# Performance work log

Measured on AMD Instinct MI355X. Metric: run time of the kernel, lower is better.

## Reference

```python
import jax, jax.numpy as jnp
import numpy as np

B, T, C = 4, 4096, 512
H, KS = 8, 9
D = C // H
PAD = KS // 2


def setup_inputs() -> dict:
    key = jax.random.key(0)
    ks = jax.random.split(key, 9)
    s = 1.0 / np.sqrt(C)
    return {
        "x": jax.random.normal(ks[0], (B, T, C), jnp.float32),
        "Wq": jax.random.normal(ks[1], (C, C), jnp.float32) * s,
        "bq": jax.random.normal(ks[2], (C,), jnp.float32) * 0.01,
        "Wk": jax.random.normal(ks[3], (C, C), jnp.float32) * s,
        "bk": jax.random.normal(ks[4], (C,), jnp.float32) * 0.01,
        "Wv": jax.random.normal(ks[5], (C, C), jnp.float32) * s,
        "bv": jax.random.normal(ks[6], (C,), jnp.float32) * 0.01,
        "Wo": jax.random.normal(ks[7], (C, C), jnp.float32) * s,
        "bo": jax.random.normal(ks[8], (C,), jnp.float32) * 0.01,
    }


def reference(x, Wq, bq, Wk, bk, Wv, bv, Wo, bo):
    Bx, Tx, Cx = x.shape
    # projections (torch Linear: x @ W.T + b), split heads -> (B,H,T,D)
    q = (x @ Wq.T + bq).reshape(Bx, Tx, H, D).transpose(0, 2, 1, 3)
    k = (x @ Wk.T + bk).reshape(Bx, Tx, H, D).transpose(0, 2, 1, 3)
    v = (x @ Wv.T + bv).reshape(Bx, Tx, H, D).transpose(0, 2, 1, 3)
    # replicate-pad along time (matches F.pad mode='replicate')
    k_pad = jnp.pad(k, ((0, 0), (0, 0), (PAD, PAD), (0, 0)), mode='edge')
    v_pad = jnp.pad(v, ((0, 0), (0, 0), (PAD, PAD), (0, 0)), mode='edge')
    # window gather indices: (T, KS) into padded time axis
    idx = jnp.arange(Tx)[:, None] + jnp.arange(KS)[None, :]
    k_unf = k_pad[:, :, idx, :]  # (B,H,T,KS,D)
    v_unf = v_pad[:, :, idx, :]  # (B,H,T,KS,D)
    scale = 1.0 / np.sqrt(D)
    scores = jnp.einsum('bhtd,bhtkd->bhtk', q, k_unf) * scale  # (B,H,T,KS)
    attn = jax.nn.softmax(scores, axis=-1)
    y = jnp.einsum('bhtk,bhtkd->bhtd', attn, v_unf)  # (B,H,T,D)
    y = y.transpose(0, 2, 1, 3).reshape(Bx, Tx, Cx)
    return y @ Wo.T + bo
```

## Files before the change

### kernel.cpp

```cpp
#include <hip/hip_runtime.h>
#include <hip/hip_bf16.h>

#define B_    4
#define T_    4096
#define C_    512
#define H_    8
#define D_    64
#define KS_   9
#define PAD_  4
#define MTOT  (B_ * T_)
#define PLANE (MTOT * C_)
#define WU    (C_ * C_ / 8)

typedef __bf16 bf16_t;
typedef __bf16 bf16x8 __attribute__((ext_vector_type(8)));
typedef float  f32x4  __attribute__((ext_vector_type(4)));

__global__ __launch_bounds__(256)
void conv_w(const float* __restrict__ Wq, const float* __restrict__ Wk,
            const float* __restrict__ Wv, const float* __restrict__ Wo,
            bf16_t* __restrict__ dst) {
  int i = blockIdx.x * 256 + threadIdx.x;
  int w = i >> 15;
  const float* W = (w == 0) ? Wq : (w == 1) ? Wk : (w == 2) ? Wv : Wo;
  const float* s = W + (size_t)(i & (WU - 1)) * 8;
  float4 f0 = ((const float4*)s)[0];
  float4 f1 = ((const float4*)s)[1];
  bf16x8 o;
  o[0] = (bf16_t)f0.x; o[1] = (bf16_t)f0.y; o[2] = (bf16_t)f0.z; o[3] = (bf16_t)f0.w;
  o[4] = (bf16_t)f1.x; o[5] = (bf16_t)f1.y; o[6] = (bf16_t)f1.z; o[7] = (bf16_t)f1.w;
  ((bf16x8*)dst)[i] = o;
}

__global__ __launch_bounds__(256, 2)
void qkv_gemm(const float* __restrict__ x, const bf16_t* __restrict__ Wb,
              const float* __restrict__ bq, const float* __restrict__ bk,
              const float* __restrict__ bv, bf16_t* __restrict__ qkv) {
  __shared__ __align__(16) bf16_t lsA[128 * 32];
  __shared__ __align__(16) bf16_t lsB[3][128 * 32];

  const int tid  = threadIdx.x;
  const int lane = tid & 63;
  const int wave = tid >> 6;
  const int wm   = (wave >> 1) * 64;
  const int wn   = (wave & 1) * 64;
  const int m0   = blockIdx.y * 128;
  const int n0   = blockIdx.x * 128;

  f32x4 acc[3][4][4] = {};

  for (int k0 = 0; k0 < C_; k0 += 32) {
    bf16x8 a[2];
#pragma unroll
    for (int s = 0; s < 2; ++s) {
      int u = s * 256 + tid;
      int row = u >> 2, slot = u & 3;
      int c = slot ^ ((row >> 1) & 3);
      const float* src = x + (size_t)(m0 + row) * C_ + k0 + c * 8;
      float4 f0 = ((const float4*)src)[0];
      float4 f1 = ((const float4*)src)[1];
      a[s][0] = (bf16_t)f0.x; a[s][1] = (bf16_t)f0.y;
      a[s][2] = (bf16_t)f0.z; a[s][3] = (bf16_t)f0.w;
      a[s][4] = (bf16_t)f1.x; a[s][5] = (bf16_t)f1.y;
      a[s][6] = (bf16_t)f1.z; a[s][7] = (bf16_t)f1.w;
    }

    __syncthreads();
    *(bf16x8*)&lsA[(size_t)tid * 8]         = a[0];
    *(bf16x8*)&lsA[(size_t)(tid + 256) * 8] = a[1];
#pragma unroll
    for (int z = 0; z < 3; ++z)
#pragma unroll
      for (int s = 0; s < 2; ++s) {
        int u = s * 256 + tid;
        int row = u >> 2, slot = u & 3;
        int c = slot ^ ((row >> 1) & 3);
        const bf16_t* gb = Wb + (size_t)z * C_ * C_ +
                           (size_t)(n0 + row) * C_ + k0 + c * 8;
        __builtin_amdgcn_global_load_lds(
            (const __attribute__((address_space(1))) unsigned int*)gb,
            (__attribute__((address_space(3))) unsigned int*)&lsB[z][u * 8],
            16, 0, 0);
      }
    __syncthreads();

    const int rr = lane & 15;
    const int q  = lane >> 4;
    const int sl = (q ^ ((rr >> 1) & 3)) << 3;
    bf16x8 af[4];
#pragma unroll
    for (int i = 0; i < 4; ++i)
      af[i] = *(const bf16x8*)&lsA[(wm + i * 16 + rr) * 32 + sl];
#pragma unroll
    for (int z = 0; z < 3; ++z) {
      bf16x8 bfr[4];
#pragma unroll
      for (int j = 0; j < 4; ++j)
        bfr[j] = *(const bf16x8*)&lsB[z][(wn + j * 16 + rr) * 32 + sl];
#pragma unroll
      for (int i = 0; i < 4; ++i)
#pragma unroll
        for (int j = 0; j < 4; ++j)
          acc[z][i][j] = __builtin_amdgcn_mfma_f32_16x16x32_bf16(
              af[i], bfr[j], acc[z][i][j], 0, 0, 0);
    }
  }

  const int cn = lane & 15;
  const int rb = (lane >> 4) << 2;
  const int bb = m0 >> 12;
  const int hh = (n0 + wn) >> 6;
#pragma unroll
  for (int z = 0; z < 3; ++z) {
    const float* bias = (z == 0) ? bq : (z == 1) ? bk : bv;
    float bvals[4];
#pragma unroll
    for (int j = 0; j < 4; ++j) bvals[j] = bias[n0 + wn + j * 16 + cn];
    bf16_t* hb = qkv + (size_t)z * PLANE + (size_t)(bb * H_ + hh) * T_ * D_;
#pragma unroll
    for (int i = 0; i < 4; ++i) {
#pragma unroll
      for (int r = 0; r < 4; ++r) {
        int t = (m0 + wm + i * 16 + rb + r) & (T_ - 1);
        bf16_t* row = hb + (size_t)t * D_;
#pragma unroll
        for (int j = 0; j < 4; ++j)
          row[j * 16 + cn] = (bf16_t)(acc[z][i][j][r] + bvals[j]);
      }
    }
  }
}

__global__ __launch_bounds__(256, 2)
void out_gemm(const bf16_t* __restrict__ y, const bf16_t* __restrict__ Wob,
              const float* __restrict__ bo, float* __restrict__ out) {
  __shared__ __align__(16) bf16_t lsA[128 * 32];
  __shared__ __align__(16) bf16_t lsB[128 * 32];

  const int tid  = threadIdx.x;
  const int lane = tid & 63;
  const int wave = tid >> 6;
  const int wm   = (wave >> 1) * 64;
  const int wn   = (wave & 1) * 64;
  const int m0   = blockIdx.y * 128;
  const int n0   = blockIdx.x * 128;

  f32x4 acc[4][4] = {};

  for (int k0 = 0; k0 < C_; k0 += 32) {
    __syncthreads();
#pragma unroll
    for (int s = 0; s < 2; ++s) {
      int u = s * 256 + tid;
      int row = u >> 2, slot = u & 3;
      int c = slot ^ ((row >> 1) & 3);
      int m = m0 + row;
      int b = m >> 12, t = m & (T_ - 1);
      int h = k0 >> 6, d0 = (k0 & 63) + c * 8;
      const bf16_t* ga = y + (((size_t)(b * H_ + h) * T_ + t) * D_ + d0);
      const bf16_t* gb = Wob + (size_t)(n0 + row) * C_ + k0 + c * 8;
      __builtin_amdgcn_global_load_lds(
          (const __attribute__((address_space(1))) unsigned int*)ga,
          (__attribute__((address_space(3))) unsigned int*)&lsA[u * 8], 16, 0, 0);
      __builtin_amdgcn_global_load_lds(
          (const __attribute__((address_space(1))) unsigned int*)gb,
          (__attribute__((address_space(3))) unsigned int*)&lsB[u * 8], 16, 0, 0);
    }
    __syncthreads();

    const int rr = lane & 15;
    const int q  = lane >> 4;
    const int sl = (q ^ ((rr >> 1) & 3)) << 3;
    bf16x8 af[4], bfr[4];
#pragma unroll
    for (int i = 0; i < 4; ++i) {
      af[i]  = *(const bf16x8*)&lsA[(wm + i * 16 + rr) * 32 + sl];
      bfr[i] = *(const bf16x8*)&lsB[(wn + i * 16 + rr) * 32 + sl];
    }
#pragma unroll
    for (int i = 0; i < 4; ++i)
#pragma unroll
      for (int j = 0; j < 4; ++j)
        acc[i][j] = __builtin_amdgcn_mfma_f32_16x16x32_bf16(af[i], bfr[j],
                                                            acc[i][j], 0, 0, 0);
  }

  const int cn = lane & 15;
  const int rb = (lane >> 4) << 2;
  float bvals[4];
#pragma unroll
  for (int j = 0; j < 4; ++j) bvals[j] = bo[n0 + wn + j * 16 + cn];
#pragma unroll
  for (int i = 0; i < 4; ++i) {
#pragma unroll
    for (int r = 0; r < 4; ++r) {
      int gm = m0 + wm + i * 16 + rb + r;
      float* orow = out + (size_t)gm * C_ + (n0 + wn);
#pragma unroll
      for (int j = 0; j < 4; ++j)
        orow[j * 16 + cn] = acc[i][j][r] + bvals[j];
    }
  }
}

__global__ __launch_bounds__(256)
void attn_kernel(const bf16_t* __restrict__ qkv, bf16_t* __restrict__ y) {
  const int tid  = threadIdx.x;
  const int sub  = tid & 7;
  const int tl   = tid >> 3;
  const int t    = blockIdx.x * 32 + tl;
  const int h    = blockIdx.y;
  const int b    = blockIdx.z;

  const size_t pl = (size_t)(b * H_ + h) * T_ * D_;
  const bf16_t* q = qkv + pl;
  const bf16_t* k = qkv + (size_t)PLANE + pl;
  const bf16_t* v = qkv + (size_t)2 * PLANE + pl;
  const int c = sub * 8;

  int tj[KS_];
#pragma unroll
  for (int j = 0; j < KS_; ++j) {
    int tt = t - PAD_ + j;
    tj[j] = tt < 0 ? 0 : (tt >= T_ ? T_ - 1 : tt);
  }

  bf16x8 q8 = *(const bf16x8*)(q + (size_t)t * D_ + c);
  float qf[8];
#pragma unroll
  for (int e = 0; e < 8; ++e) qf[e] = (float)q8[e];

  float s[KS_];
#pragma unroll
  for (int j = 0; j < KS_; ++j) {
    bf16x8 k8 = *(const bf16x8*)(k + (size_t)tj[j] * D_ + c);
    float d0 = 0.f;
#pragma unroll
    for (int e = 0; e < 8; ++e) d0 += qf[e] * (float)k8[e];
    s[j] = d0;
  }

#pragma unroll
  for (int m = 1; m < 8; m <<= 1)
#pragma unroll
    for (int j = 0; j < KS_; ++j) s[j] += __shfl_xor(s[j], m, 8);

  float mx = s[0];
#pragma unroll
  for (int j = 1; j < KS_; ++j) mx = fmaxf(mx, s[j]);
  float w[KS_], sum = 0.f;
#pragma unroll
  for (int j = 0; j < KS_; ++j) {
    w[j] = __expf((s[j] - mx) * 0.125f);
    sum += w[j];
  }
  const float inv = 1.f / sum;
#pragma unroll
  for (int j = 0; j < KS_; ++j) w[j] *= inv;

  float o[8] = {0.f, 0.f, 0.f, 0.f, 0.f, 0.f, 0.f, 0.f};
#pragma unroll
  for (int j = 0; j < KS_; ++j) {
    bf16x8 v8 = *(const bf16x8*)(v + (size_t)tj[j] * D_ + c);
#pragma unroll
    for (int e = 0; e < 8; ++e) o[e] += w[j] * (float)v8[e];
  }
  bf16x8 o8;
#pragma unroll
  for (int e = 0; e < 8; ++e) o8[e] = (bf16_t)o[e];
  *(bf16x8*)(y + pl + (size_t)t * D_ + c) = o8;
}

extern "C" void kernel_launch(void* const* d_in, const int* in_sizes, int n_in,
                              void* d_out, int out_size, void* d_ws, size_t ws_size,
                              hipStream_t stream) {
  const float* x  = (const float*)d_in[0];
  const float* Wq = (const float*)d_in[1];
  const float* bq = (const float*)d_in[2];
  const float* Wk = (const float*)d_in[3];
  const float* bk = (const float*)d_in[4];
  const float* Wv = (const float*)d_in[5];
  const float* bv = (const float*)d_in[6];
  const float* Wo = (const float*)d_in[7];
  const float* bo = (const float*)d_in[8];
  float* out = (float*)d_out;

  bf16_t* Wb  = (bf16_t*)d_ws;
  bf16_t* qkv = Wb + (size_t)4 * C_ * C_;
  bf16_t* y   = qkv + (size_t)3 * PLANE;

  conv_w<<<4 * WU / 256, 256, 0, stream>>>(Wq, Wk, Wv, Wo, Wb);
  qkv_gemm<<<dim3(C_ / 128, MTOT / 128), 256, 0, stream>>>(
      x, Wb, bq, bk, bv, qkv);
  attn_kernel<<<dim3(T_ / 32, H_, B_), 256, 0, stream>>>(qkv, y);
  out_gemm<<<dim3(C_ / 128, MTOT / 128, 1), 256, 0, stream>>>(
      y, Wb + (size_t)3 * C_ * C_, bo, out);
}
```

Baseline: 168.1 us.

## Replace QKV and output GEMMs with a triple-buffered 256x128 pipelined GEMM

Converts x to bf16 in the same pre-pass that converts the weights, then runs both projections through one templated GEMM. The GEMM uses 512-thread blocks, 256x128x64 tiles, three LDS stages fed by direct global-to-LDS loads, interleaved MFMA/load phases with barriers and priority hints, and an XCD-aware block remap. The goal is to hide memory latency and raise MFMA utilisation compared with the old single-buffered 128x128x32 kernels. The cost is an extra bf16 copy of x written to workspace, which is then reused as the attention output buffer, and much more intricate synchronisation.

```diff
diff --git a/kernel.cpp b/kernel.cpp
--- a/kernel.cpp
+++ b/kernel.cpp
@@ -17,188 +17,233 @@
 typedef float  f32x4  __attribute__((ext_vector_type(4)));
 
 __global__ __launch_bounds__(256)
-void conv_w(const float* __restrict__ Wq, const float* __restrict__ Wk,
-            const float* __restrict__ Wv, const float* __restrict__ Wo,
-            bf16_t* __restrict__ dst) {
+void conv_all(const float* __restrict__ Wq, const float* __restrict__ Wk,
+              const float* __restrict__ Wv, const float* __restrict__ Wo,
+              const float* __restrict__ x,
+              bf16_t* __restrict__ Wb, bf16_t* __restrict__ xb) {
   int i = blockIdx.x * 256 + threadIdx.x;
-  int w = i >> 15;
-  const float* W = (w == 0) ? Wq : (w == 1) ? Wk : (w == 2) ? Wv : Wo;
-  const float* s = W + (size_t)(i & (WU - 1)) * 8;
-  float4 f0 = ((const float4*)s)[0];
-  float4 f1 = ((const float4*)s)[1];
+  const float* src;
+  bf16_t* dst;
+  if (i < 4 * WU) {
+    int w = i >> 15;
+    const float* W = (w == 0) ? Wq : (w == 1) ? Wk : (w == 2) ? Wv : Wo;
+    src = W + (size_t)(i & (WU - 1)) * 8;
+    dst = Wb + (size_t)i * 8;
+  } else {
+    size_t j = (size_t)(i - 4 * WU);
+    src = x + j * 8;
+    dst = xb + j * 8;
+  }
+  float4 f0 = ((const float4*)src)[0];
+  float4 f1 = ((const float4*)src)[1];
   bf16x8 o;
   o[0] = (bf16_t)f0.x; o[1] = (bf16_t)f0.y; o[2] = (bf16_t)f0.z; o[3] = (bf16_t)f0.w;
   o[4] = (bf16_t)f1.x; o[5] = (bf16_t)f1.y; o[6] = (bf16_t)f1.z; o[7] = (bf16_t)f1.w;
-  ((bf16x8*)dst)[i] = o;
+  *(bf16x8*)dst = o;
 }
 
-__global__ __launch_bounds__(256, 2)
-void qkv_gemm(const float* __restrict__ x, const bf16_t* __restrict__ Wb,
-              const float* __restrict__ bq, const float* __restrict__ bk,
-              const float* __restrict__ bv, bf16_t* __restrict__ qkv) {
-  __shared__ __align__(16) bf16_t lsA[128 * 32];
-  __shared__ __align__(16) bf16_t lsB[3][128 * 32];
+#define BM   256
+#define BN   128
+#define BK   64
+#define NKT  (C_ / BK)
+#define ASL  (BM * BK)
+#define BSL  (BN * BK)
+#define SLOT (ASL + BSL)
+
+#define GLD(srcp, off) __builtin_amdgcn_global_load_lds(                     \
+    (const __attribute__((address_space(1))) unsigned int*)(srcp),           \
+    (__attribute__((address_space(3))) unsigned int*)(&sm[off]), 16, 0, 0)
+
+template<int MODE>
+__global__ __launch_bounds__(512, 2)
+void gemm8p(const bf16_t* __restrict__ A, const bf16_t* __restrict__ Bw,
+            const float* __restrict__ b0, const float* __restrict__ b1,
+            const float* __restrict__ b2, void* __restrict__ Outp) {
+  __shared__ __align__(16) bf16_t sm[3 * SLOT];
+
+  constexpr int GX  = (MODE == 0) ? (3 * C_ / BN) : (C_ / BN);
+  constexpr int NWG = GX * (MTOT / BM);
+  constexpr int CPX = NWG / 8;
+
+  const int ord = blockIdx.y * GX + blockIdx.x;
+  const int lg  = (ord & 7) * CPX + (ord >> 3);
+  const int n0  = (lg % GX) * BN;
+  const int m0  = (lg / GX) * BM;
 
   const int tid  = threadIdx.x;
   const int lane = tid & 63;
   const int wave = tid >> 6;
-  const int wm   = (wave >> 1) * 64;
-  const int wn   = (wave & 1) * 64;
-  const int m0   = blockIdx.y * 128;
-  const int n0   = blockIdx.x * 128;
-
-  f32x4 acc[3][4][4] = {};
-
-  for (int k0 = 0; k0 < C_; k0 += 32) {
-    bf16x8 a[2];
-#pragma unroll
-    for (int s = 0; s < 2; ++s) {
-      int u = s * 256 + tid;
-      int row = u >> 2, slot = u & 3;
-      int c = slot ^ ((row >> 1) & 3);
-      const float* src = x + (size_t)(m0 + row) * C_ + k0 + c * 8;
-      float4 f0 = ((const float4*)src)[0];
-      float4 f1 = ((const float4*)src)[1];
-      a[s][0] = (bf16_t)f0.x; a[s][1] = (bf16_t)f0.y;
-      a[s][2] = (bf16_t)f0.z; a[s][3] = (bf16_t)f0.w;
-      a[s][4] = (bf16_t)f1.x; a[s][5] = (bf16_t)f1.y;
-      a[s][6] = (bf16_t)f1.z; a[s][7] = (bf16_t)f1.w;
-    }
-
-    __syncthreads();
-    *(bf16x8*)&lsA[(size_t)tid * 8]         = a[0];
-    *(bf16x8*)&lsA[(size_t)(tid + 256) * 8] = a[1];
-#pragma unroll
-    for (int z = 0; z < 3; ++z)
-#pragma unroll
-      for (int s = 0; s < 2; ++s) {
-        int u = s * 256 + tid;
-        int row = u >> 2, slot = u & 3;
-        int c = slot ^ ((row >> 1) & 3);
-        const bf16_t* gb = Wb + (size_t)z * C_ * C_ +
-                           (size_t)(n0 + row) * C_ + k0 + c * 8;
-        __builtin_amdgcn_global_load_lds(
-            (const __attribute__((address_space(1))) unsigned int*)gb,
-            (__attribute__((address_space(3))) unsigned int*)&lsB[z][u * 8],
-            16, 0, 0);
-      }
-    __syncthreads();
-
-    const int rr = lane & 15;
-    const int q  = lane >> 4;
-    const int sl = (q ^ ((rr >> 1) & 3)) << 3;
-    bf16x8 af[4];
+  const int wm   = wave >> 2;
+  const int wn   = wave & 3;
+
+  const bf16_t* aSrc[4];
+  const bf16_t* bSrc[2];
+#pragma unroll
+  for (int s = 0; s < 4; ++s) {
+    int u = s * 512 + tid, r = u >> 3, ch = u & 7;
+    int cs = (ch ^ (r & 7)) << 3;
+    if (MODE == 0) {
+      aSrc[s] = A + (size_t)(m0 + r) * C_ + cs;
+    } else {
+      int bb = m0 >> 12, t0 = m0 & (T_ - 1);
+      aSrc[s] = A + ((size_t)bb * H_ * T_ + t0 + r) * D_ + cs;
+    }
+  }
+#pragma unroll
+  for (int s = 0; s < 2; ++s) {
+    int u = s * 512 + tid, r = u >> 3, ch = u & 7;
+    int cs = (ch ^ (r & 7)) << 3;
+    bSrc[s] = Bw + (size_t)(n0 + r) * C_ + cs;
+  }
+  constexpr size_t ASTEP = (MODE == 0) ? (size_t)BK : (size_t)T_ * D_;
+
+#pragma unroll
+  for (int s = 0; s < 4; ++s) GLD(aSrc[s], (s * 512 + tid) * 8);
+#pragma unroll
+  for (int s = 0; s < 2; ++s) GLD(bSrc[s], ASL + (s * 512 + tid) * 8);
+#pragma unroll
+  for (int s = 0; s < 4; ++s) GLD(aSrc[s] + ASTEP, SLOT + (s * 512 + tid) * 8);
+#pragma unroll
+  for (int s = 0; s < 2; ++s) GLD(bSrc[s] + BK, SLOT + ASL + (s * 512 + tid) * 8);
+  asm volatile("s_waitcnt vmcnt(6)" ::: "memory");
+  __builtin_amdgcn_s_barrier();
+
+  f32x4 acc[8][2] = {};
+  const int lr  = lane & 15;
+  const int lq  = lane >> 4;
+  const int co0 = ((0 + lq) ^ (lane & 7)) << 3;
+  const int co1 = ((4 + lq) ^ (lane & 7)) << 3;
+
+  int rsl = 0;
+  for (int kt = 0; kt < NKT; ++kt) {
+    const bf16_t* arow = &sm[rsl * SLOT + (wm * 128 + lr) * 64];
+    const bf16_t* brow = &sm[rsl * SLOT + ASL + (wn * 32 + lr) * 64];
+    const int  wof = ((rsl == 0) ? 2 : rsl - 1) * SLOT;
+    const bool st  = (kt + 2 < NKT);
+    const size_t ka = (size_t)(kt + 2) * ASTEP;
+    const size_t kb = (size_t)(kt + 2) * BK;
+
+    bf16x8 af[4][2], bfr[2][2];
+
+#pragma unroll
+    for (int i = 0; i < 4; ++i) {
+      af[i][0] = *(const bf16x8*)(arow + i * 1024 + co0);
+      af[i][1] = *(const bf16x8*)(arow + i * 1024 + co1);
+    }
+#pragma unroll
+    for (int nf = 0; nf < 2; ++nf) {
+      bfr[nf][0] = *(const bf16x8*)(brow + nf * 1024 + co0);
+      bfr[nf][1] = *(const bf16x8*)(brow + nf * 1024 + co1);
+    }
+    if (st) {
+      GLD(aSrc[0] + ka, wof + (0 * 512 + tid) * 8);
+      GLD(aSrc[1] + ka, wof + (1 * 512 + tid) * 8);
+    }
+    __builtin_amdgcn_sched_barrier(0);
+    __builtin_amdgcn_s_barrier();
+    asm volatile("s_waitcnt lgkmcnt(0)" ::: "memory");
+    __builtin_amdgcn_sched_barrier(0);
+    __builtin_amdgcn_s_setprio(1);
 #pragma unroll
     for (int i = 0; i < 4; ++i)
-      af[i] = *(const bf16x8*)&lsA[(wm + i * 16 + rr) * 32 + sl];
-#pragma unroll
-    for (int z = 0; z < 3; ++z) {
-      bf16x8 bfr[4];
-#pragma unroll
-      for (int j = 0; j < 4; ++j)
-        bfr[j] = *(const bf16x8*)&lsB[z][(wn + j * 16 + rr) * 32 + sl];
-#pragma unroll
-      for (int i = 0; i < 4; ++i)
-#pragma unroll
-        for (int j = 0; j < 4; ++j)
-          acc[z][i][j] = __builtin_amdgcn_mfma_f32_16x16x32_bf16(
-              af[i], bfr[j], acc[z][i][j], 0, 0, 0);
-    }
-  }
-
-  const int cn = lane & 15;
-  const int rb = (lane >> 4) << 2;
-  const int bb = m0 >> 12;
-  const int hh = (n0 + wn) >> 6;
-#pragma unroll
-  for (int z = 0; z < 3; ++z) {
-    const float* bias = (z == 0) ? bq : (z == 1) ? bk : bv;
-    float bvals[4];
-#pragma unroll
-    for (int j = 0; j < 4; ++j) bvals[j] = bias[n0 + wn + j * 16 + cn];
-    bf16_t* hb = qkv + (size_t)z * PLANE + (size_t)(bb * H_ + hh) * T_ * D_;
+#pragma unroll
+      for (int kk = 0; kk < 2; ++kk)
+        acc[i][0] = __builtin_amdgcn_mfma_f32_16x16x32_bf16(
+            af[i][kk], bfr[0][kk], acc[i][0], 0, 0, 0);
+    __builtin_amdgcn_s_setprio(0);
+    __builtin_amdgcn_sched_barrier(0);
+    __builtin_amdgcn_s_barrier();
+
+    if (st) {
+      GLD(aSrc[2] + ka, wof + (2 * 512 + tid) * 8);
+      GLD(aSrc[3] + ka, wof + (3 * 512 + tid) * 8);
+    }
+    __builtin_amdgcn_sched_barrier(0);
+    __builtin_amdgcn_s_barrier();
+    __builtin_amdgcn_s_setprio(1);
+#pragma unroll
+    for (int i = 0; i < 4; ++i)
+#pragma unroll
+      for (int kk = 0; kk < 2; ++kk)
+        acc[i][1] = __builtin_amdgcn_mfma_f32_16x16x32_bf16(
+            af[i][kk], bfr[1][kk], acc[i][1], 0, 0, 0);
+    __builtin_amdgcn_s_setprio(0);
+    __builtin_amdgcn_sched_barrier(0);
+    __builtin_amdgcn_s_barrier();
+
 #pragma unroll
     for (int i = 0; i < 4; ++i) {
-#pragma unroll
-      for (int r = 0; r < 4; ++r) {
-        int t = (m0 + wm + i * 16 + rb + r) & (T_ - 1);
-        bf16_t* row = hb + (size_t)t * D_;
-#pragma unroll
-        for (int j = 0; j < 4; ++j)
-          row[j * 16 + cn] = (bf16_t)(acc[z][i][j][r] + bvals[j]);
-      }
-    }
-  }
-}
-
-__global__ __launch_bounds__(256, 2)
-void out_gemm(const bf16_t* __restrict__ y, const bf16_t* __restrict__ Wob,
-              const float* __restrict__ bo, float* __restrict__ out) {
-  __shared__ __align__(16) bf16_t lsA[128 * 32];
-  __shared__ __align__(16) bf16_t lsB[128 * 32];
-
-  const int tid  = threadIdx.x;
-  const int lane = tid & 63;
-  const int wave = tid >> 6;
-  const int wm   = (wave >> 1) * 64;
-  const int wn   = (wave & 1) * 64;
-  const int m0   = blockIdx.y * 128;
-  const int n0   = blockIdx.x * 128;
-
-  f32x4 acc[4][4] = {};
-
-  for (int k0 = 0; k0 < C_; k0 += 32) {
-    __syncthreads();
-#pragma unroll
-    for (int s = 0; s < 2; ++s) {
-      int u = s * 256 + tid;
-      int row = u >> 2, slot = u & 3;
-      int c = slot ^ ((row >> 1) & 3);
-      int m = m0 + row;
-      int b = m >> 12, t = m & (T_ - 1);
-      int h = k0 >> 6, d0 = (k0 & 63) + c * 8;
-      const bf16_t* ga = y + (((size_t)(b * H_ + h) * T_ + t) * D_ + d0);
-      const bf16_t* gb = Wob + (size_t)(n0 + row) * C_ + k0 + c * 8;
-      __builtin_amdgcn_global_load_lds(
-          (const __attribute__((address_space(1))) unsigned int*)ga,
-          (__attribute__((address_space(3))) unsigned int*)&lsA[u * 8], 16, 0, 0);
-      __builtin_amdgcn_global_load_lds(
-          (const __attribute__((address_space(1))) unsigned int*)gb,
-          (__attribute__((address_space(3))) unsigned int*)&lsB[u * 8], 16, 0, 0);
-    }
-    __syncthreads();
-
-    const int rr = lane & 15;
-    const int q  = lane >> 4;
-    const int sl = (q ^ ((rr >> 1) & 3)) << 3;
-    bf16x8 af[4], bfr[4];
-#pragma unroll
-    for (int i = 0; i < 4; ++i) {
-      af[i]  = *(const bf16x8*)&lsA[(wm + i * 16 + rr) * 32 + sl];
-      bfr[i] = *(const bf16x8*)&lsB[(wn + i * 16 + rr) * 32 + sl];
-    }
+      af[i][0] = *(const bf16x8*)(arow + 4096 + i * 1024 + co0);
+      af[i][1] = *(const bf16x8*)(arow + 4096 + i * 1024 + co1);
+    }
+    if (st) {
+      GLD(bSrc[0] + kb, wof + ASL + (0 * 512 + tid) * 8);
+      GLD(bSrc[1] + kb, wof + ASL + (1 * 512 + tid) * 8);
+    }
+    __builtin_amdgcn_sched_barrier(0);
+    __builtin_amdgcn_s_barrier();
+    asm volatile("s_waitcnt lgkmcnt(0)" ::: "memory");
+    __builtin_amdgcn_sched_barrier(0);
+    __builtin_amdgcn_s_setprio(1);
 #pragma unroll
     for (int i = 0; i < 4; ++i)
 #pragma unroll
-      for (int j = 0; j < 4; ++j)
-        acc[i][j] = __builtin_amdgcn_mfma_f32_16x16x32_bf16(af[i], bfr[j],
-                                                            acc[i][j], 0, 0, 0);
-  }
-
-  const int cn = lane & 15;
-  const int rb = (lane >> 4) << 2;
-  float bvals[4];
-#pragma unroll
-  for (int j = 0; j < 4; ++j) bvals[j] = bo[n0 + wn + j * 16 + cn];
-#pragma unroll
-  for (int i = 0; i < 4; ++i) {
-#pragma unroll
-    for (int r = 0; r < 4; ++r) {
-      int gm = m0 + wm + i * 16 + rb + r;
-      float* orow = out + (size_t)gm * C_ + (n0 + wn);
-#pragma unroll
-      for (int j = 0; j < 4; ++j)
-        orow[j * 16 + cn] = acc[i][j][r] + bvals[j];
+      for (int kk = 0; kk < 2; ++kk)
+        acc[4 + i][0] = __builtin_amdgcn_mfma_f32_16x16x32_bf16(
+            af[i][kk], bfr[0][kk], acc[4 + i][0], 0, 0, 0);
+    __builtin_amdgcn_s_setprio(0);
+    __builtin_amdgcn_sched_barrier(0);
+    __builtin_amdgcn_s_barrier();
+
+    __builtin_amdgcn_s_setprio(1);
+#pragma unroll
+    for (int i = 0; i < 4; ++i)
+#pragma unroll
+      for (int kk = 0; kk < 2; ++kk)
+        acc[4 + i][1] = __builtin_amdgcn_mfma_f32_16x16x32_bf16(
+            af[i][kk], bfr[1][kk], acc[4 + i][1], 0, 0, 0);
+    __builtin_amdgcn_s_setprio(0);
+    __builtin_amdgcn_sched_barrier(0);
+    if (kt < NKT - 2)       asm volatile("s_waitcnt vmcnt(6)" ::: "memory");
+    else if (kt == NKT - 2) asm volatile("s_waitcnt vmcnt(0)" ::: "memory");
+    __builtin_amdgcn_s_barrier();
+    rsl = (rsl == 2) ? 0 : rsl + 1;
+  }
+
+  const int rq = (lane >> 4) << 2;
+  if constexpr (MODE == 0) {
+    const int z  = n0 >> 9;
+    const float* bias = (z == 0) ? b0 : (z == 1) ? b1 : b2;
+    const int bb = m0 >> 12;
+    const int t0 = m0 & (T_ - 1);
+    bf16_t* plane = (bf16_t*)Outp + (size_t)z * PLANE;
+#pragma unroll
+    for (int nf = 0; nf < 2; ++nf) {
+      const int cc  = (n0 & (C_ - 1)) + wn * 32 + nf * 16 + lr;
+      const int hh  = cc >> 6, dd = cc & 63;
+      const float bvv = bias[cc];
+      bf16_t* hb = plane + ((size_t)(bb * H_ + hh) * T_) * D_ + dd;
+#pragma unroll
+      for (int f = 0; f < 8; ++f)
+#pragma unroll
+        for (int r = 0; r < 4; ++r) {
+          const int t = t0 + wm * 128 + f * 16 + rq + r;
+          hb[(size_t)t * D_] = (bf16_t)(acc[f][nf][r] + bvv);
+        }
+    }
+  } else {
+    float* outp = (float*)Outp;
+#pragma unroll
+    for (int nf = 0; nf < 2; ++nf) {
+      const int n = n0 + wn * 32 + nf * 16 + lr;
+      const float bvv = b0[n];
+#pragma unroll
+      for (int f = 0; f < 8; ++f)
+#pragma unroll
+        for (int r = 0; r < 4; ++r) {
+          const int m = m0 + wm * 128 + f * 16 + rq + r;
+          outp[(size_t)m * C_ + n] = acc[f][nf][r] + bvv;
+        }
     }
   }
 }
@@ -286,13 +331,14 @@
   float* out = (float*)d_out;
 
   bf16_t* Wb  = (bf16_t*)d_ws;
-  bf16_t* qkv = Wb + (size_t)4 * C_ * C_;
-  bf16_t* y   = qkv + (size_t)3 * PLANE;
-
-  conv_w<<<4 * WU / 256, 256, 0, stream>>>(Wq, Wk, Wv, Wo, Wb);
-  qkv_gemm<<<dim3(C_ / 128, MTOT / 128), 256, 0, stream>>>(
-      x, Wb, bq, bk, bv, qkv);
+  bf16_t* xb  = Wb + (size_t)4 * C_ * C_;
+  bf16_t* qkv = xb + (size_t)PLANE;
+  bf16_t* y   = xb;
+
+  conv_all<<<(4 * WU + PLANE / 8) / 256, 256, 0, stream>>>(Wq, Wk, Wv, Wo, x, Wb, xb);
+  gemm8p<0><<<dim3(3 * C_ / BN, MTOT / BM), 512, 0, stream>>>(
+      xb, Wb, bq, bk, bv, qkv);
   attn_kernel<<<dim3(T_ / 32, H_, B_), 256, 0, stream>>>(qkv, y);
-  out_gemm<<<dim3(C_ / 128, MTOT / 128, 1), 256, 0, stream>>>(
-      y, Wb + (size_t)3 * C_ * C_, bo, out);
+  gemm8p<1><<<dim3(C_ / BN, MTOT / BM), 512, 0, stream>>>(
+      y, Wb + (size_t)3 * C_ * C_, bo, nullptr, nullptr, out);
 }
```

New measurement: 167.9 us. Within noise of the previous version (-0.1%).
